# Kernel tuning notes

Measured on AMD Instinct MI355X. Metric: run time of the kernel, lower is better.

Reference implementation:

```python
import jax, jax.numpy as jnp
import numpy as np

EMBED_DIM = 1024
NUM_HEADS = 16
HEAD_DIM = EMBED_DIM // NUM_HEADS


def setup_inputs() -> dict:
    key = jax.random.key(0)
    k_x, k_wqkv, k_bqkv, k_wp, k_bp = jax.random.split(key, 5)
    B, N, C = 4, 2048, EMBED_DIM
    bound_qkv = 1.0 / np.sqrt(C)
    bound_p = 1.0 / np.sqrt(C)
    return {
        "x": jax.random.normal(k_x, (B, N, C), dtype=jnp.float32),
        # nn.Linear stores weight as [out, in]; we keep that layout and use x @ W.T
        "w_qkv": jax.random.uniform(k_wqkv, (3 * C, C), jnp.float32, -bound_qkv, bound_qkv),
        "b_qkv": jax.random.uniform(k_bqkv, (3 * C,), jnp.float32, -bound_qkv, bound_qkv),
        "w_proj": jax.random.uniform(k_wp, (C, C), jnp.float32, -bound_p, bound_p),
        "b_proj": jax.random.uniform(k_bp, (C,), jnp.float32, -bound_p, bound_p),
    }


def reference(x, w_qkv, b_qkv, w_proj, b_proj):
    B, N, C = x.shape
    H, D = NUM_HEADS, HEAD_DIM
    qkv = x @ w_qkv.T + b_qkv                      # [B, N, 3C]
    qkv = qkv.reshape(B, N, 3, H, D)
    q = qkv[:, :, 0].transpose(0, 2, 1, 3)          # [B, H, N, D]
    k = qkv[:, :, 1].transpose(0, 2, 1, 3)
    v = qkv[:, :, 2].transpose(0, 2, 1, 3)
    scale = jnp.asarray(D, x.dtype) ** -0.5
    attn = jnp.einsum('bhqd,bhkd->bhqk', q, k) * scale  # [B, H, N, N]
    attn = jax.nn.softmax(attn, axis=-1)
    out = jnp.einsum('bhqk,bhkd->bhqd', attn, v)        # [B, H, N, D]
    out = out.transpose(0, 2, 1, 3).reshape(B, N, C)
    return out @ w_proj.T + b_proj
```

## Files before the change

### kernel.cpp

```cpp
#include <hip/hip_runtime.h>

typedef unsigned short u16;
typedef __attribute__((ext_vector_type(8))) short short8;
typedef __attribute__((ext_vector_type(4))) short s16x4;
typedef __attribute__((ext_vector_type(8))) _Float16 half8;
typedef __attribute__((ext_vector_type(4))) float f32x4;
typedef __attribute__((ext_vector_type(16))) float f32x16;
typedef __attribute__((ext_vector_type(4))) unsigned int u32x4;

#define DEVI static __device__ __forceinline__

static constexpr int B_ = 4, N_ = 2048, C_ = 1024, H_ = 16, D_ = 64;
static constexpr int M_ = B_ * N_;
static constexpr int C3 = 3072;

DEVI u16 f2h(float f) {
  _Float16 h = (_Float16)f;
  return __builtin_bit_cast(u16, h);
}

DEVI unsigned pk2h(float lo, float hi) {
  return __builtin_bit_cast(unsigned, __builtin_amdgcn_cvt_pkrtz(lo, hi));
}

DEVI void gload_lds16(const void* g, void* lds) {
  __builtin_amdgcn_global_load_lds(
      (const __attribute__((address_space(1))) unsigned int*)g,
      (__attribute__((address_space(3))) unsigned int*)lds, 16, 0, 0);
}

__global__ __launch_bounds__(256) void f32_to_f16_all(const float* __restrict__ x,
                                                      const float* __restrict__ wq,
                                                      const float* __restrict__ wp,
                                                      u16* __restrict__ x16,
                                                      u16* __restrict__ wq16,
                                                      u16* __restrict__ wp16) {
  int idx = blockIdx.x * 256 + threadIdx.x;
  const float* s;
  u16* d;
  int base;
  if (idx < 1048576) {
    s = x; d = x16; base = idx;
  } else if (idx < 1048576 + 393216) {
    s = wq; d = wq16; base = idx - 1048576;
  } else {
    s = wp; d = wp16; base = idx - 1441792;
  }
  const float* sp = s + (size_t)base * 8;
  f32x4 f0 = *(const f32x4*)sp;
  f32x4 f1 = *(const f32x4*)(sp + 4);
  short8 o;
#pragma unroll
  for (int j = 0; j < 8; ++j) o[j] = (short)f2h(j < 4 ? f0[j] : f1[j - 4]);
  *(short8*)(d + (size_t)base * 8) = o;
}

template <bool OUT_F16>
__global__ __launch_bounds__(256) void gemm_bt(const u16* __restrict__ A,
                                               const u16* __restrict__ Bm,
                                               const float* __restrict__ bias,
                                               void* __restrict__ outp, int Nout) {
  __shared__ u16 As[128 * 64];
  __shared__ u16 Bs[128 * 64];
  const int tid = threadIdx.x;
  const int w = tid >> 6, l = tid & 63;
  const int wr = w >> 1, wc = w & 1;
  const int l15 = l & 15, lg = l >> 4;
  const int e7 = l15 & 7;
  const int nx = gridDim.x;
  int bid = blockIdx.y * nx + blockIdx.x;
  int cpx = (nx * gridDim.y) >> 3;
  int swz = (bid & 7) * cpx + (bid >> 3);
  int bx = swz % nx, by = swz / nx;
  const u16* Ab = A + (size_t)(bx * 128) * C_;
  const u16* Bb = Bm + (size_t)(by * 128) * C_;
  const int srow = tid >> 3;
  const int sgc8 = (((tid & 7) ^ ((tid >> 3) & 7)) * 8);
  const int fc0 = (lg ^ e7) << 4;
  const int fc1 = ((4 + lg) ^ e7) << 4;
  f32x4 acc[4][4];
#pragma unroll
  for (int m = 0; m < 4; ++m)
#pragma unroll
    for (int n = 0; n < 4; ++n) acc[m][n] = (f32x4){0.f, 0.f, 0.f, 0.f};

  for (int kt = 0; kt < C_; kt += 64) {
    __syncthreads();
#pragma unroll
    for (int i = 0; i < 4; ++i) {
      int r = i * 32 + srow;
      gload_lds16(Ab + (size_t)r * C_ + kt + sgc8, (char*)As + i * 4096 + w * 1024);
      gload_lds16(Bb + (size_t)r * C_ + kt + sgc8, (char*)Bs + i * 4096 + w * 1024);
    }
    __syncthreads();
#pragma unroll
    for (int kk = 0; kk < 2; ++kk) {
      const int fco = kk ? fc1 : fc0;
      half8 af[4], bf[4];
#pragma unroll
      for (int m = 0; m < 4; ++m)
        af[m] = __builtin_bit_cast(half8, *(const short8*)((const char*)As +
                    (wr * 64 + m * 16 + l15) * 128 + fco));
#pragma unroll
      for (int n = 0; n < 4; ++n)
        bf[n] = __builtin_bit_cast(half8, *(const short8*)((const char*)Bs +
                    (wc * 64 + n * 16 + l15) * 128 + fco));
#pragma unroll
      for (int m = 0; m < 4; ++m)
#pragma unroll
        for (int n = 0; n < 4; ++n)
          acc[m][n] = __builtin_amdgcn_mfma_f32_16x16x32_f16(af[m], bf[n], acc[m][n], 0, 0, 0);
    }
  }
#pragma unroll
  for (int m = 0; m < 4; ++m)
#pragma unroll
    for (int n = 0; n < 4; ++n) {
      int col = by * 128 + wc * 64 + n * 16 + l15;
      float bval = bias[col];
#pragma unroll
      for (int i = 0; i < 4; ++i) {
        int row = bx * 128 + wr * 64 + m * 16 + lg * 4 + i;
        float v = acc[m][n][i] + bval;
        if (OUT_F16)
          ((u16*)outp)[(size_t)row * Nout + col] = f2h(v);
        else
          ((float*)outp)[(size_t)row * Nout + col] = v;
      }
    }
}

__global__ __launch_bounds__(256) void kv_prep(const u16* __restrict__ qkv,
                                               u16* __restrict__ kf,
                                               u16* __restrict__ vf) {
  __shared__ u16 tile[64][72];
  const int bxk = blockIdx.x;
  if (bxk < 4096) {
    int g = bxk * 256 + threadIdx.x;
    int l = g & 63;
    int df = (g >> 6) & 3;
    int kh = (g >> 8) & 1;
    int t = (g >> 9) & 31;
    int bh = g >> 14;
    int b = bh >> 4, h = bh & 15;
    const u16* src = qkv + (size_t)(b * N_ + t * 64 + kh * 32 + (l & 31)) * C3 +
                     C_ + h * D_ + (df * 2 + (l >> 5)) * 8;
    *(short8*)(kf + (size_t)g * 8) = *(const short8*)src;
    return;
  }
  const int idx2 = bxk - 4096;
  const int t = idx2 & 31, bh = idx2 >> 5;
  const int b = bh >> 4, h = bh & 15;
  const int tid = threadIdx.x;
  const int r = tid >> 3, c8 = (tid & 7) * 8;
#pragma unroll
  for (int rr = 0; rr < 2; ++rr) {
    int row = rr * 32 + r;
    short8 v = *(const short8*)(qkv + (size_t)(b * N_ + t * 64 + row) * C3 +
                                2 * C_ + h * D_ + c8);
    *(short8*)&tile[row][c8] = v;
  }
  __syncthreads();
  const int l = tid & 63, wv = tid >> 6;
  const int l31 = l & 31, hi = l >> 5;
#pragma unroll
  for (int i = 0; i < 2; ++i) {
    int combo = wv * 2 + i;
    int vh = combo >> 2, kc = combo & 3;
    short8 o;
#pragma unroll
    for (int jj = 0; jj < 8; ++jj)
      o[jj] = (short)tile[kc * 16 + (jj & 3) + 8 * (jj >> 2) + 4 * hi][vh * 32 + l31];
    *(short8*)(vf + ((size_t)(bh * 32 + t) * 8 + combo) * 512 + l * 8) = o;
  }
}

__global__ __launch_bounds__(256, 2) void attn_fused(const u16* __restrict__ qkv,
                                                     const u16* __restrict__ kf,
                                                     const u16* __restrict__ vf,
                                                     u16* __restrict__ att) {
  __shared__ float red[2][64][68];
  const int tid = threadIdx.x;
  const int w = tid >> 6, l = tid & 63;
  const int l31 = l & 31, hi = l >> 5;
  const int qg = w >> 1, kvh = w & 1;
  int bid = blockIdx.y * gridDim.x + blockIdx.x;
  int swz = (bid & 7) * 128 + (bid >> 3);
  const int qt = swz & 15, bh = swz >> 4;
  const int b = bh >> 4, h = bh & 15;
  const int qb = qt * 128 + qg * 64;

  const float sc2 = 0.125f * 1.4426950408889634f;
  half8 qfA[4], qfB[4];
  {
    const _Float16 sch = (_Float16)sc2;
    const u16* qrowA = qkv + (size_t)(b * N_ + qb + l31) * C3 + h * D_ + hi * 8;
    const u16* qrowB = qrowA + (size_t)32 * C3;
#pragma unroll
    for (int df = 0; df < 4; ++df) {
      half8 qa = __builtin_bit_cast(half8, *(const short8*)(qrowA + df * 16));
      half8 qc = __builtin_bit_cast(half8, *(const short8*)(qrowB + df * 16));
#pragma unroll
      for (int j = 0; j < 8; ++j) { qa[j] *= sch; qc[j] *= sch; }
      qfA[df] = qa;
      qfB[df] = qc;
    }
  }

  f32x16 aA0, aA1, aB0, aB1;
#pragma unroll
  for (int j = 0; j < 16; ++j) { aA0[j] = 0.f; aA1[j] = 0.f; aB0[j] = 0.f; aB1[j] = 0.f; }
  float lrowA = 0.f, lrowB = 0.f;

  const u16* kp = kf + (size_t)bh * 32 * 4096;
  const u16* vp = vf + (size_t)bh * 32 * 4096;
  const int loff = l * 8;

#define MKPF(SV, J0, OUT)                                                      \
  {                                                                            \
    u32x4 wq = {pk2h(SV[J0 + 0], SV[J0 + 1]), pk2h(SV[J0 + 2], SV[J0 + 3]),   \
                pk2h(SV[J0 + 4], SV[J0 + 5]), pk2h(SV[J0 + 6], SV[J0 + 7])};   \
    OUT = __builtin_bit_cast(half8, wq);                                       \
  }

  const int t0 = kvh * 16;
  const int trot = qg * 8;
  for (int i = 0; i < 16; ++i) {
    const int t = t0 + ((i + trot) & 15);
    const u16* kt = kp + t * 4096;
    const u16* vt = vp + t * 4096;

    half8 kfr[2][4];
#pragma unroll
    for (int kh = 0; kh < 2; ++kh)
#pragma unroll
      for (int df = 0; df < 4; ++df)
        kfr[kh][df] = __builtin_bit_cast(half8,
            *(const short8*)(kt + ((kh * 4 + df) * 64) * 8 + loff));

    f32x16 sA0, sA1;
#pragma unroll
    for (int j = 0; j < 16; ++j) { sA0[j] = 0.f; sA1[j] = 0.f; }
#pragma unroll
    for (int df = 0; df < 4; ++df) {
      sA0 = __builtin_amdgcn_mfma_f32_32x32x16_f16(kfr[0][df], qfA[df], sA0, 0, 0, 0);
      sA1 = __builtin_amdgcn_mfma_f32_32x32x16_f16(kfr[1][df], qfA[df], sA1, 0, 0, 0);
    }
    float suA[4] = {0.f, 0.f, 0.f, 0.f};
#pragma unroll
    for (int j = 0; j < 16; ++j) {
      sA0[j] = __builtin_amdgcn_exp2f(sA0[j]);
      suA[j & 3] += sA0[j];
    }
#pragma unroll
    for (int j = 0; j < 16; ++j) {
      sA1[j] = __builtin_amdgcn_exp2f(sA1[j]);
      suA[j & 3] += sA1[j];
    }
    lrowA += (suA[0] + suA[1]) + (suA[2] + suA[3]);
    half8 pfA0, pfA1, pfA2, pfA3;
    MKPF(sA0, 0, pfA0)
    MKPF(sA0, 8, pfA1)
    MKPF(sA1, 0, pfA2)
    MKPF(sA1, 8, pfA3)

    f32x16 sB0, sB1;
#pragma unroll
    for (int j = 0; j < 16; ++j) { sB0[j] = 0.f; sB1[j] = 0.f; }
#pragma unroll
    for (int df = 0; df < 4; ++df) {
      sB0 = __builtin_amdgcn_mfma_f32_32x32x16_f16(kfr[0][df], qfB[df], sB0, 0, 0, 0);
      sB1 = __builtin_amdgcn_mfma_f32_32x32x16_f16(kfr[1][df], qfB[df], sB1, 0, 0, 0);
    }

    half8 vfr[2][4];
#pragma unroll
    for (int vh = 0; vh < 2; ++vh)
#pragma unroll
      for (int kc = 0; kc < 4; ++kc)
        vfr[vh][kc] = __builtin_bit_cast(half8,
            *(const short8*)(vt + ((vh * 4 + kc) * 64) * 8 + loff));

    float suB[4] = {0.f, 0.f, 0.f, 0.f};
#pragma unroll
    for (int j = 0; j < 16; ++j) {
      sB0[j] = __builtin_amdgcn_exp2f(sB0[j]);
      suB[j & 3] += sB0[j];
    }
#pragma unroll
    for (int j = 0; j < 16; ++j) {
      sB1[j] = __builtin_amdgcn_exp2f(sB1[j]);
      suB[j & 3] += sB1[j];
    }
    lrowB += (suB[0] + suB[1]) + (suB[2] + suB[3]);
    half8 pfB0, pfB1, pfB2, pfB3;
    MKPF(sB0, 0, pfB0)
    MKPF(sB0, 8, pfB1)
    MKPF(sB1, 0, pfB2)
    MKPF(sB1, 8, pfB3)

    aA0 = __builtin_amdgcn_mfma_f32_32x32x16_f16(vfr[0][0], pfA0, aA0, 0, 0, 0);
    aA1 = __builtin_amdgcn_mfma_f32_32x32x16_f16(vfr[1][0], pfA0, aA1, 0, 0, 0);
    aB0 = __builtin_amdgcn_mfma_f32_32x32x16_f16(vfr[0][0], pfB0, aB0, 0, 0, 0);
    aB1 = __builtin_amdgcn_mfma_f32_32x32x16_f16(vfr[1][0], pfB0, aB1, 0, 0, 0);
    aA0 = __builtin_amdgcn_mfma_f32_32x32x16_f16(vfr[0][1], pfA1, aA0, 0, 0, 0);
    aA1 = __builtin_amdgcn_mfma_f32_32x32x16_f16(vfr[1][1], pfA1, aA1, 0, 0, 0);
    aB0 = __builtin_amdgcn_mfma_f32_32x32x16_f16(vfr[0][1], pfB1, aB0, 0, 0, 0);
    aB1 = __builtin_amdgcn_mfma_f32_32x32x16_f16(vfr[1][1], pfB1, aB1, 0, 0, 0);
    aA0 = __builtin_amdgcn_mfma_f32_32x32x16_f16(vfr[0][2], pfA2, aA0, 0, 0, 0);
    aA1 = __builtin_amdgcn_mfma_f32_32x32x16_f16(vfr[1][2], pfA2, aA1, 0, 0, 0);
    aB0 = __builtin_amdgcn_mfma_f32_32x32x16_f16(vfr[0][2], pfB2, aB0, 0, 0, 0);
    aB1 = __builtin_amdgcn_mfma_f32_32x32x16_f16(vfr[1][2], pfB2, aB1, 0, 0, 0);
    aA0 = __builtin_amdgcn_mfma_f32_32x32x16_f16(vfr[0][3], pfA3, aA0, 0, 0, 0);
    aA1 = __builtin_amdgcn_mfma_f32_32x32x16_f16(vfr[1][3], pfA3, aA1, 0, 0, 0);
    aB0 = __builtin_amdgcn_mfma_f32_32x32x16_f16(vfr[0][3], pfB3, aB0, 0, 0, 0);
    aB1 = __builtin_amdgcn_mfma_f32_32x32x16_f16(vfr[1][3], pfB3, aB1, 0, 0, 0);
  }
#undef MKPF

  if (kvh) {
    float* s = &red[qg][l][0];
#pragma unroll
    for (int j = 0; j < 16; ++j) {
      s[j] = aA0[j];
      s[16 + j] = aA1[j];
      s[32 + j] = aB0[j];
      s[48 + j] = aB1[j];
    }
    s[64] = lrowA;
    s[65] = lrowB;
  }
  __syncthreads();
  if (!kvh) {
    const float* s = &red[qg][l][0];
#pragma unroll
    for (int j = 0; j < 16; ++j) {
      aA0[j] += s[j];
      aA1[j] += s[16 + j];
      aB0[j] += s[32 + j];
      aB1[j] += s[48 + j];
    }
    lrowA += s[64];
    lrowB += s[65];

    lrowA += __shfl_xor(lrowA, 32);
    lrowB += __shfl_xor(lrowB, 32);
    float rinvA = 1.0f / lrowA;
    float rinvB = 1.0f / lrowB;
    u16* orowA = att + (size_t)(b * N_ + qb + l31) * C_ + h * D_;
    u16* orowB = orowA + (size_t)32 * C_;
#pragma unroll
    for (int dt = 0; dt < 2; ++dt) {
#pragma unroll
      for (int r2 = 0; r2 < 4; ++r2) {
        int d0 = dt * 32 + r2 * 8 + hi * 4;
        s16x4 hvA, hvB;
#pragma unroll
        for (int i = 0; i < 4; ++i) {
          float vA = (dt ? aA1[r2 * 4 + i] : aA0[r2 * 4 + i]) * rinvA;
          float vB = (dt ? aB1[r2 * 4 + i] : aB0[r2 * 4 + i]) * rinvB;
          hvA[i] = (short)f2h(vA);
          hvB[i] = (short)f2h(vB);
        }
        *(s16x4*)(orowA + d0) = hvA;
        *(s16x4*)(orowB + d0) = hvB;
      }
    }
  }
}

extern "C" void kernel_launch(void* const* d_in, const int* in_sizes, int n_in,
                              void* d_out, int out_size, void* d_ws, size_t ws_size,
                              hipStream_t stream) {
  const float* x = (const float*)d_in[0];
  const float* w_qkv = (const float*)d_in[1];
  const float* b_qkv = (const float*)d_in[2];
  const float* w_proj = (const float*)d_in[3];
  const float* b_proj = (const float*)d_in[4];

  char* ws = (char*)d_ws;
  u16* qkv  = (u16*)(ws + 0);
  u16* x16  = (u16*)(ws + 50331648);
  u16* wq16 = (u16*)(ws + 67108864);
  u16* wp16 = (u16*)(ws + 73400320);
  u16* kf   = (u16*)(ws + 75497472);
  u16* vf   = (u16*)(ws + 92274688);
  u16* att  = (u16*)(ws + 109051904);

  f32_to_f16_all<<<6144, 256, 0, stream>>>(x, w_qkv, w_proj, x16, wq16, wp16);

  gemm_bt<true><<<dim3(64, 24), 256, 0, stream>>>(x16, wq16, b_qkv, qkv, C3);

  kv_prep<<<6144, 256, 0, stream>>>(qkv, kf, vf);

  attn_fused<<<dim3(16, 64), 256, 0, stream>>>(qkv, kf, vf, att);

  gemm_bt<false><<<dim3(64, 8), 256, 0, stream>>>(att, wp16, b_proj, d_out, C_);
}
```

Baseline: 201.4 us.

## Fuse K/V layout prep into QKV GEMM epilogue and drop split-KV reduction

```diff
diff --git a/kernel.cpp b/kernel.cpp
--- a/kernel.cpp
+++ b/kernel.cpp
@@ -55,11 +55,12 @@
   *(short8*)(d + (size_t)base * 8) = o;
 }
 
-template <bool OUT_F16>
-__global__ __launch_bounds__(256) void gemm_bt(const u16* __restrict__ A,
-                                               const u16* __restrict__ Bm,
-                                               const float* __restrict__ bias,
-                                               void* __restrict__ outp, int Nout) {
+__global__ __launch_bounds__(256) void gemm_qkv(const u16* __restrict__ A,
+                                                const u16* __restrict__ Bm,
+                                                const float* __restrict__ bias,
+                                                u16* __restrict__ q16,
+                                                u16* __restrict__ kf,
+                                                u16* __restrict__ vf) {
   __shared__ u16 As[128 * 64];
   __shared__ u16 Bs[128 * 64];
   const int tid = threadIdx.x;
@@ -112,90 +113,154 @@
           acc[m][n] = __builtin_amdgcn_mfma_f32_16x16x32_f16(af[m], bf[n], acc[m][n], 0, 0, 0);
     }
   }
-#pragma unroll
-  for (int m = 0; m < 4; ++m)
+
+  if (by < 8) {
 #pragma unroll
     for (int n = 0; n < 4; ++n) {
       int col = by * 128 + wc * 64 + n * 16 + l15;
       float bval = bias[col];
 #pragma unroll
+      for (int m = 0; m < 4; ++m)
+#pragma unroll
+        for (int i = 0; i < 4; ++i) {
+          int row = bx * 128 + wr * 64 + m * 16 + lg * 4 + i;
+          q16[(size_t)row * C_ + col] = f2h(acc[m][n][i] + bval);
+        }
+    }
+  } else if (by < 16) {
+#pragma unroll
+    for (int n = 0; n < 4; ++n) {
+      int col = by * 128 + wc * 64 + n * 16 + l15;
+      float bval = bias[col];
+      int ck = col - 1024;
+      int h = ck >> 6, d = ck & 63;
+      int s = d >> 3, df = s >> 1, hi2 = s & 1, e = d & 7;
+#pragma unroll
+      for (int m = 0; m < 4; ++m)
+#pragma unroll
+        for (int i = 0; i < 4; ++i) {
+          int row = bx * 128 + wr * 64 + m * 16 + lg * 4 + i;
+          int b = row >> 11, kg = row & 2047;
+          int t = kg >> 6, kin = kg & 63, kh = kin >> 5, l31k = kin & 31;
+          size_t addr = (((((size_t)(b * 16 + h) * 32 + t) * 2 + kh) * 4 + df) * 64 +
+                         hi2 * 32 + l31k) * 8 + e;
+          kf[addr] = f2h(acc[m][n][i] + bval);
+        }
+    }
+  } else {
+#pragma unroll
+    for (int n = 0; n < 4; ++n) {
+      int col = by * 128 + wc * 64 + n * 16 + l15;
+      float bval = bias[col];
+      int cv = col - 2048;
+      int h = cv >> 6, d = cv & 63;
+      int vh = d >> 5, l31v = d & 31;
+#pragma unroll
+      for (int m = 0; m < 4; ++m)
+#pragma unroll
+        for (int i = 0; i < 4; ++i) {
+          int row = bx * 128 + wr * 64 + m * 16 + lg * 4 + i;
+          int b = row >> 11, kg = row & 2047;
+          int t = kg >> 6, kin = kg & 63, kc = kin >> 4, k16 = kin & 15;
+          int jj = (k16 & 3) + 4 * (k16 >> 3);
+          int hi2 = (k16 >> 2) & 1;
+          size_t addr = ((((size_t)(b * 16 + h) * 32 + t) * 8 + vh * 4 + kc) * 64 +
+                         hi2 * 32 + l31v) * 8 + jj;
+          vf[addr] = f2h(acc[m][n][i] + bval);
+        }
+    }
+  }
+}
+
+__global__ __launch_bounds__(256) void gemm_bt(const u16* __restrict__ A,
+                                               const u16* __restrict__ Bm,
+                                               const float* __restrict__ bias,
+                                               float* __restrict__ outp, int Nout) {
+  __shared__ u16 As[128 * 64];
+  __shared__ u16 Bs[128 * 64];
+  const int tid = threadIdx.x;
+  const int w = tid >> 6, l = tid & 63;
+  const int wr = w >> 1, wc = w & 1;
+  const int l15 = l & 15, lg = l >> 4;
+  const int e7 = l15 & 7;
+  const int nx = gridDim.x;
+  int bid = blockIdx.y * nx + blockIdx.x;
+  int cpx = (nx * gridDim.y) >> 3;
+  int swz = (bid & 7) * cpx + (bid >> 3);
+  int bx = swz % nx, by = swz / nx;
+  const u16* Ab = A + (size_t)(bx * 128) * C_;
+  const u16* Bb = Bm + (size_t)(by * 128) * C_;
+  const int srow = tid >> 3;
+  const int sgc8 = (((tid & 7) ^ ((tid >> 3) & 7)) * 8);
+  const int fc0 = (lg ^ e7) << 4;
+  const int fc1 = ((4 + lg) ^ e7) << 4;
+  f32x4 acc[4][4];
+#pragma unroll
+  for (int m = 0; m < 4; ++m)
+#pragma unroll
+    for (int n = 0; n < 4; ++n) acc[m][n] = (f32x4){0.f, 0.f, 0.f, 0.f};
+
+  for (int kt = 0; kt < C_; kt += 64) {
+    __syncthreads();
+#pragma unroll
+    for (int i = 0; i < 4; ++i) {
+      int r = i * 32 + srow;
+      gload_lds16(Ab + (size_t)r * C_ + kt + sgc8, (char*)As + i * 4096 + w * 1024);
+      gload_lds16(Bb + (size_t)r * C_ + kt + sgc8, (char*)Bs + i * 4096 + w * 1024);
+    }
+    __syncthreads();
+#pragma unroll
+    for (int kk = 0; kk < 2; ++kk) {
+      const int fco = kk ? fc1 : fc0;
+      half8 af[4], bf[4];
+#pragma unroll
+      for (int m = 0; m < 4; ++m)
+        af[m] = __builtin_bit_cast(half8, *(const short8*)((const char*)As +
+                    (wr * 64 + m * 16 + l15) * 128 + fco));
+#pragma unroll
+      for (int n = 0; n < 4; ++n)
+        bf[n] = __builtin_bit_cast(half8, *(const short8*)((const char*)Bs +
+                    (wc * 64 + n * 16 + l15) * 128 + fco));
+#pragma unroll
+      for (int m = 0; m < 4; ++m)
+#pragma unroll
+        for (int n = 0; n < 4; ++n)
+          acc[m][n] = __builtin_amdgcn_mfma_f32_16x16x32_f16(af[m], bf[n], acc[m][n], 0, 0, 0);
+    }
+  }
+#pragma unroll
+  for (int m = 0; m < 4; ++m)
+#pragma unroll
+    for (int n = 0; n < 4; ++n) {
+      int col = by * 128 + wc * 64 + n * 16 + l15;
+      float bval = bias[col];
+#pragma unroll
       for (int i = 0; i < 4; ++i) {
         int row = bx * 128 + wr * 64 + m * 16 + lg * 4 + i;
-        float v = acc[m][n][i] + bval;
-        if (OUT_F16)
-          ((u16*)outp)[(size_t)row * Nout + col] = f2h(v);
-        else
-          ((float*)outp)[(size_t)row * Nout + col] = v;
+        outp[(size_t)row * Nout + col] = acc[m][n][i] + bval;
       }
     }
 }
 
-__global__ __launch_bounds__(256) void kv_prep(const u16* __restrict__ qkv,
-                                               u16* __restrict__ kf,
-                                               u16* __restrict__ vf) {
-  __shared__ u16 tile[64][72];
-  const int bxk = blockIdx.x;
-  if (bxk < 4096) {
-    int g = bxk * 256 + threadIdx.x;
-    int l = g & 63;
-    int df = (g >> 6) & 3;
-    int kh = (g >> 8) & 1;
-    int t = (g >> 9) & 31;
-    int bh = g >> 14;
-    int b = bh >> 4, h = bh & 15;
-    const u16* src = qkv + (size_t)(b * N_ + t * 64 + kh * 32 + (l & 31)) * C3 +
-                     C_ + h * D_ + (df * 2 + (l >> 5)) * 8;
-    *(short8*)(kf + (size_t)g * 8) = *(const short8*)src;
-    return;
-  }
-  const int idx2 = bxk - 4096;
-  const int t = idx2 & 31, bh = idx2 >> 5;
-  const int b = bh >> 4, h = bh & 15;
-  const int tid = threadIdx.x;
-  const int r = tid >> 3, c8 = (tid & 7) * 8;
-#pragma unroll
-  for (int rr = 0; rr < 2; ++rr) {
-    int row = rr * 32 + r;
-    short8 v = *(const short8*)(qkv + (size_t)(b * N_ + t * 64 + row) * C3 +
-                                2 * C_ + h * D_ + c8);
-    *(short8*)&tile[row][c8] = v;
-  }
-  __syncthreads();
-  const int l = tid & 63, wv = tid >> 6;
-  const int l31 = l & 31, hi = l >> 5;
-#pragma unroll
-  for (int i = 0; i < 2; ++i) {
-    int combo = wv * 2 + i;
-    int vh = combo >> 2, kc = combo & 3;
-    short8 o;
-#pragma unroll
-    for (int jj = 0; jj < 8; ++jj)
-      o[jj] = (short)tile[kc * 16 + (jj & 3) + 8 * (jj >> 2) + 4 * hi][vh * 32 + l31];
-    *(short8*)(vf + ((size_t)(bh * 32 + t) * 8 + combo) * 512 + l * 8) = o;
-  }
-}
-
-__global__ __launch_bounds__(256, 2) void attn_fused(const u16* __restrict__ qkv,
+__global__ __launch_bounds__(256, 2) void attn_fused(const u16* __restrict__ q16,
                                                      const u16* __restrict__ kf,
                                                      const u16* __restrict__ vf,
                                                      u16* __restrict__ att) {
-  __shared__ float red[2][64][68];
   const int tid = threadIdx.x;
   const int w = tid >> 6, l = tid & 63;
   const int l31 = l & 31, hi = l >> 5;
-  const int qg = w >> 1, kvh = w & 1;
   int bid = blockIdx.y * gridDim.x + blockIdx.x;
-  int swz = (bid & 7) * 128 + (bid >> 3);
-  const int qt = swz & 15, bh = swz >> 4;
+  int swz = (bid & 7) * 64 + (bid >> 3);
+  const int qt = swz & 7, bh = swz >> 3;
   const int b = bh >> 4, h = bh & 15;
-  const int qb = qt * 128 + qg * 64;
+  const int qb = qt * 256 + w * 64;
 
   const float sc2 = 0.125f * 1.4426950408889634f;
   half8 qfA[4], qfB[4];
   {
     const _Float16 sch = (_Float16)sc2;
-    const u16* qrowA = qkv + (size_t)(b * N_ + qb + l31) * C3 + h * D_ + hi * 8;
-    const u16* qrowB = qrowA + (size_t)32 * C3;
+    const u16* qrowA = q16 + (size_t)(b * N_ + qb + l31) * C_ + h * D_ + hi * 8;
+    const u16* qrowB = qrowA + (size_t)32 * C_;
 #pragma unroll
     for (int df = 0; df < 4; ++df) {
       half8 qa = __builtin_bit_cast(half8, *(const short8*)(qrowA + df * 16));
@@ -223,10 +288,7 @@
     OUT = __builtin_bit_cast(half8, wq);                                       \
   }
 
-  const int t0 = kvh * 16;
-  const int trot = qg * 8;
-  for (int i = 0; i < 16; ++i) {
-    const int t = t0 + ((i + trot) & 15);
+  for (int t = 0; t < 32; ++t) {
     const u16* kt = kp + t * 4096;
     const u16* vt = vp + t * 4096;
 
@@ -241,11 +303,13 @@
     f32x16 sA0, sA1;
 #pragma unroll
     for (int j = 0; j < 16; ++j) { sA0[j] = 0.f; sA1[j] = 0.f; }
+    __builtin_amdgcn_s_setprio(1);
 #pragma unroll
     for (int df = 0; df < 4; ++df) {
       sA0 = __builtin_amdgcn_mfma_f32_32x32x16_f16(kfr[0][df], qfA[df], sA0, 0, 0, 0);
       sA1 = __builtin_amdgcn_mfma_f32_32x32x16_f16(kfr[1][df], qfA[df], sA1, 0, 0, 0);
     }
+    __builtin_amdgcn_s_setprio(0);
     float suA[4] = {0.f, 0.f, 0.f, 0.f};
 #pragma unroll
     for (int j = 0; j < 16; ++j) {
@@ -267,11 +331,13 @@
     f32x16 sB0, sB1;
 #pragma unroll
     for (int j = 0; j < 16; ++j) { sB0[j] = 0.f; sB1[j] = 0.f; }
+    __builtin_amdgcn_s_setprio(1);
 #pragma unroll
     for (int df = 0; df < 4; ++df) {
       sB0 = __builtin_amdgcn_mfma_f32_32x32x16_f16(kfr[0][df], qfB[df], sB0, 0, 0, 0);
       sB1 = __builtin_amdgcn_mfma_f32_32x32x16_f16(kfr[1][df], qfB[df], sB1, 0, 0, 0);
     }
+    __builtin_amdgcn_s_setprio(0);
 
     half8 vfr[2][4];
 #pragma unroll
@@ -299,6 +365,7 @@
     MKPF(sB1, 0, pfB2)
     MKPF(sB1, 8, pfB3)
 
+    __builtin_amdgcn_s_setprio(1);
     aA0 = __builtin_amdgcn_mfma_f32_32x32x16_f16(vfr[0][0], pfA0, aA0, 0, 0, 0);
     aA1 = __builtin_amdgcn_mfma_f32_32x32x16_f16(vfr[1][0], pfA0, aA1, 0, 0, 0);
     aB0 = __builtin_amdgcn_mfma_f32_32x32x16_f16(vfr[0][0], pfB0, aB0, 0, 0, 0);
@@ -315,34 +382,11 @@
     aA1 = __builtin_amdgcn_mfma_f32_32x32x16_f16(vfr[1][3], pfA3, aA1, 0, 0, 0);
     aB0 = __builtin_amdgcn_mfma_f32_32x32x16_f16(vfr[0][3], pfB3, aB0, 0, 0, 0);
     aB1 = __builtin_amdgcn_mfma_f32_32x32x16_f16(vfr[1][3], pfB3, aB1, 0, 0, 0);
+    __builtin_amdgcn_s_setprio(0);
   }
 #undef MKPF
 
-  if (kvh) {
-    float* s = &red[qg][l][0];
-#pragma unroll
-    for (int j = 0; j < 16; ++j) {
-      s[j] = aA0[j];
-      s[16 + j] = aA1[j];
-      s[32 + j] = aB0[j];
-      s[48 + j] = aB1[j];
-    }
-    s[64] = lrowA;
-    s[65] = lrowB;
-  }
-  __syncthreads();
-  if (!kvh) {
-    const float* s = &red[qg][l][0];
-#pragma unroll
-    for (int j = 0; j < 16; ++j) {
-      aA0[j] += s[j];
-      aA1[j] += s[16 + j];
-      aB0[j] += s[32 + j];
-      aB1[j] += s[48 + j];
-    }
-    lrowA += s[64];
-    lrowB += s[65];
-
+  {
     lrowA += __shfl_xor(lrowA, 32);
     lrowB += __shfl_xor(lrowB, 32);
     float rinvA = 1.0f / lrowA;
@@ -379,21 +423,19 @@
   const float* b_proj = (const float*)d_in[4];
 
   char* ws = (char*)d_ws;
-  u16* qkv  = (u16*)(ws + 0);
-  u16* x16  = (u16*)(ws + 50331648);
-  u16* wq16 = (u16*)(ws + 67108864);
-  u16* wp16 = (u16*)(ws + 73400320);
-  u16* kf   = (u16*)(ws + 75497472);
-  u16* vf   = (u16*)(ws + 92274688);
-  u16* att  = (u16*)(ws + 109051904);
+  u16* q16  = (u16*)(ws + 0);
+  u16* x16  = (u16*)(ws + 16777216);
+  u16* wq16 = (u16*)(ws + 33554432);
+  u16* wp16 = (u16*)(ws + 39845888);
+  u16* kf   = (u16*)(ws + 41943040);
+  u16* vf   = (u16*)(ws + 58720256);
+  u16* att  = (u16*)(ws + 75497472);
 
   f32_to_f16_all<<<6144, 256, 0, stream>>>(x, w_qkv, w_proj, x16, wq16, wp16);
 
-  gemm_bt<true><<<dim3(64, 24), 256, 0, stream>>>(x16, wq16, b_qkv, qkv, C3);
-
-  kv_prep<<<6144, 256, 0, stream>>>(qkv, kf, vf);
-
-  attn_fused<<<dim3(16, 64), 256, 0, stream>>>(qkv, kf, vf, att);
-
-  gemm_bt<false><<<dim3(64, 8), 256, 0, stream>>>(att, wp16, b_proj, d_out, C_);
-}
+  gemm_qkv<<<dim3(64, 24), 256, 0, stream>>>(x16, wq16, b_qkv, q16, kf, vf);
+
+  attn_fused<<<dim3(8, 64), 256, 0, stream>>>(q16, kf, vf, att);
+
+  gemm_bt<<<dim3(64, 8), 256, 0, stream>>>(att, wp16, b_proj, (float*)d_out, C_);
+}
```

After: 195.6 us. 2.9% less time.
